# Kernel tuning notes

Hardware: AMD Instinct MI355X
Metric: run time of the kernel (lower is better)

The kernel has to match this reference:

```python
import jax, jax.numpy as jnp
import numpy as np

N = 1_000_000   # total nodes
D = 128         # hidden_dim
B = 1024        # number of graphs (segments)
E = 2_000_000   # edges (unused by forward math, kept for signature fidelity)
EPS = 1e-16     # PyG softmax denominator epsilon


def setup_inputs() -> dict:
    key = jax.random.key(0)
    k1, k2, k3, k4 = jax.random.split(key, 4)
    x = jax.random.normal(k1, (N, D), dtype=jnp.float32)
    edge_index = jax.random.randint(k2, (2, E), 0, N, dtype=jnp.int32)
    batch = jnp.sort(jax.random.randint(k3, (N,), 0, B, dtype=jnp.int32))
    # Linear(hidden_dim, 1) parameters
    W = jax.random.normal(k4, (1, D), dtype=jnp.float32) * (1.0 / np.sqrt(D))
    b = jnp.zeros((1,), dtype=jnp.float32)
    return {"x": x, "edge_index": edge_index, "batch": batch, "W": W, "b": b}


def reference(x, edge_index, batch, W, b):
    # scores = Linear(x).squeeze(-1)  -> [N]
    scores = (x @ W.T + b)[:, 0]
    # pyg_softmax: segment-wise numerically-stable softmax over `batch`
    seg_max = jax.ops.segment_max(scores, batch, num_segments=B)          # [B]
    ex = jnp.exp(scores - seg_max[batch])                                  # [N]
    seg_sum = jax.ops.segment_sum(ex, batch, num_segments=B)              # [B]
    attn = ex / (seg_sum[batch] + EPS)                                     # [N]
    # global_add_pool of attention-weighted features -> [B, D]
    gx = jax.ops.segment_sum(x * attn[:, None], batch, num_segments=B)
    return gx
```

## Files before the change

### kernel.cpp

```cpp
#include <hip/hip_runtime.h>
#include <math.h>


#define DIM 128

__device__ __forceinline__ int lower_bound_i32(const int* __restrict__ a, int n, int key) {
    int lo = 0, hi = n;
    while (lo < hi) {
        int mid = (lo + hi) >> 1;
        if (a[mid] < key) lo = mid + 1; else hi = mid;
    }
    return lo;
}

__global__ __launch_bounds__(256) void gap_online_kernel(
    const float* __restrict__ x,
    const int*   __restrict__ batch,
    const float* __restrict__ W,
    const float* __restrict__ bias,
    float*       __restrict__ out,
    int N)
{
    const int seg  = blockIdx.x;
    const int tid  = threadIdx.x;
    const int wave = tid >> 6;
    const int lane = tid & 63;

    const int start = lower_bound_i32(batch, N, seg);
    const int end   = lower_bound_i32(batch, N, seg + 1);

    const float2 wv = ((const float2*)W)[lane];
    const float  b0 = bias[0];

    float  m   = -INFINITY;
    float  l   = 0.0f;
    float2 acc = make_float2(0.0f, 0.0f);

    for (int r = start + wave; r < end; r += 4) {
        const float2 xv = ((const float2*)(x + (size_t)r * DIM))[lane];

        float s = xv.x * wv.x + xv.y * wv.y;
        #pragma unroll
        for (int off = 32; off > 0; off >>= 1)
            s += __shfl_xor(s, off, 64);
        s += b0;

        const float m_new = fmaxf(m, s);
        const float alpha = __expf(m - m_new);
        const float w     = __expf(s - m_new);
        l     = l * alpha + w;
        acc.x = acc.x * alpha + w * xv.x;
        acc.y = acc.y * alpha + w * xv.y;
        m     = m_new;
    }

    __shared__ float sm[4];
    __shared__ float sl[4];
    __shared__ float sacc[4][DIM];

    sacc[wave][2 * lane]     = acc.x;
    sacc[wave][2 * lane + 1] = acc.y;
    if (lane == 0) { sm[wave] = m; sl[wave] = l; }
    __syncthreads();

    if (tid < DIM) {
        float m_tot = fmaxf(fmaxf(sm[0], sm[1]), fmaxf(sm[2], sm[3]));
        float num = 0.0f, den = 0.0f;
        #pragma unroll
        for (int w = 0; w < 4; ++w) {
            const float a = (sl[w] > 0.0f) ? __expf(sm[w] - m_tot) : 0.0f;
            num += sacc[w][tid] * a;
            den += sl[w] * a;
        }
        out[(size_t)seg * DIM + tid] = (den > 0.0f) ? (num / (den + 1e-16f)) : 0.0f;
    }
}

extern "C" void kernel_launch(void* const* d_in, const int* in_sizes, int n_in,
                              void* d_out, int out_size, void* d_ws, size_t ws_size,
                              hipStream_t stream) {
    const float* x     = (const float*)d_in[0];
    const int*   batch = (const int*)d_in[2];
    const float* W     = (const float*)d_in[3];
    const float* bias  = (const float*)d_in[4];
    float*       out   = (float*)d_out;

    const int N = in_sizes[2];
    const int B = out_size / DIM;

    gap_online_kernel<<<B, 256, 0, stream>>>(x, batch, W, bias, out, N);
}
```

Measured before the change: 749.8 us.

## Precompute segment offsets and use float4 half-wave rows with prefetch

Replaces the per-block binary searches over batch with a separate kernel that writes segment offsets into workspace. The main kernel now has each half-wave handle one row using float4 loads, so a wave covers two rows per step. Each wave processes 8 rows per iteration and register-prefetches the next group to raise memory-level parallelism. The cost is an extra launch plus a pass over batch. The empty-segment guards are removed, with a large negative sentinel used in place of -inf.

```diff
diff --git a/kernel.cpp b/kernel.cpp
--- a/kernel.cpp
+++ b/kernel.cpp
@@ -3,76 +3,117 @@
 
 
 #define DIM 128
+#define NEG_HUGE (-3.0e38f)
 
-__device__ __forceinline__ int lower_bound_i32(const int* __restrict__ a, int n, int key) {
-    int lo = 0, hi = n;
-    while (lo < hi) {
-        int mid = (lo + hi) >> 1;
-        if (a[mid] < key) lo = mid + 1; else hi = mid;
+__global__ void seg_offsets_kernel(const int* __restrict__ batch,
+                                   int* __restrict__ off, int N, int B) {
+    int i = blockIdx.x * blockDim.x + threadIdx.x;
+    if (i >= N) return;
+    int bi = batch[i];
+    int bp = (i == 0) ? -1 : batch[i - 1];
+    for (int s = bp + 1; s <= bi; ++s) off[s] = i;
+    if (i == N - 1) {
+        for (int s = bi + 1; s <= B; ++s) off[s] = N;
     }
-    return lo;
 }
 
 __global__ __launch_bounds__(256) void gap_online_kernel(
     const float* __restrict__ x,
-    const int*   __restrict__ batch,
+    const int*   __restrict__ off,
     const float* __restrict__ W,
     const float* __restrict__ bias,
-    float*       __restrict__ out,
-    int N)
+    float*       __restrict__ out)
 {
     const int seg  = blockIdx.x;
     const int tid  = threadIdx.x;
     const int wave = tid >> 6;
     const int lane = tid & 63;
+    const int half = lane >> 5;
+    const int hl   = lane & 31;
 
-    const int start = lower_bound_i32(batch, N, seg);
-    const int end   = lower_bound_i32(batch, N, seg + 1);
+    const int start = off[seg];
+    const int end   = off[seg + 1];
 
-    const float2 wv = ((const float2*)W)[lane];
+    const float4 wv = ((const float4*)W)[hl];
     const float  b0 = bias[0];
 
-    float  m   = -INFINITY;
-    float  l   = 0.0f;
-    float2 acc = make_float2(0.0f, 0.0f);
+    float  m = NEG_HUGE;
+    float  l = 0.0f;
+    float4 acc = make_float4(0.f, 0.f, 0.f, 0.f);
 
-    for (int r = start + wave; r < end; r += 4) {
-        const float2 xv = ((const float2*)(x + (size_t)r * DIM))[lane];
+    int p = start + wave * 8;
 
-        float s = xv.x * wv.x + xv.y * wv.y;
-        #pragma unroll
-        for (int off = 32; off > 0; off >>= 1)
-            s += __shfl_xor(s, off, 64);
-        s += b0;
-
-        const float m_new = fmaxf(m, s);
-        const float alpha = __expf(m - m_new);
-        const float w     = __expf(s - m_new);
-        l     = l * alpha + w;
-        acc.x = acc.x * alpha + w * xv.x;
-        acc.y = acc.y * alpha + w * xv.y;
-        m     = m_new;
+    float4 xv[4];
+    #pragma unroll
+    for (int k = 0; k < 4; ++k) {
+        int row = p + 2 * k + half;
+        xv[k] = (row < end) ? ((const float4*)(x + (size_t)row * DIM))[hl]
+                            : make_float4(0.f, 0.f, 0.f, 0.f);
     }
 
-    __shared__ float sm[4];
-    __shared__ float sl[4];
-    __shared__ float sacc[4][DIM];
+    for (; p < end; p += 32) {
+        float4 xn[4];
+        #pragma unroll
+        for (int k = 0; k < 4; ++k) {
+            int row = p + 32 + 2 * k + half;
+            xn[k] = (row < end) ? ((const float4*)(x + (size_t)row * DIM))[hl]
+                                : make_float4(0.f, 0.f, 0.f, 0.f);
+        }
 
-    sacc[wave][2 * lane]     = acc.x;
-    sacc[wave][2 * lane + 1] = acc.y;
-    if (lane == 0) { sm[wave] = m; sl[wave] = l; }
+        float s[4];
+        #pragma unroll
+        for (int k = 0; k < 4; ++k)
+            s[k] = xv[k].x * wv.x + xv[k].y * wv.y + xv[k].z * wv.z + xv[k].w * wv.w;
+
+        #pragma unroll
+        for (int offd = 16; offd > 0; offd >>= 1) {
+            #pragma unroll
+            for (int k = 0; k < 4; ++k)
+                s[k] += __shfl_xor(s[k], offd, 64);
+        }
+
+        #pragma unroll
+        for (int k = 0; k < 4; ++k) {
+            int  row   = p + 2 * k + half;
+            bool valid = row < end;
+            float sk    = valid ? (s[k] + b0) : NEG_HUGE;
+            float m_new = fmaxf(m, sk);
+            float alpha = __expf(m - m_new);
+            float w     = valid ? __expf(sk - m_new) : 0.0f;
+            l     = l * alpha + w;
+            acc.x = acc.x * alpha + w * xv[k].x;
+            acc.y = acc.y * alpha + w * xv[k].y;
+            acc.z = acc.z * alpha + w * xv[k].z;
+            acc.w = acc.w * alpha + w * xv[k].w;
+            m     = m_new;
+            xv[k] = xn[k];
+        }
+    }
+
+    __shared__ float sm[8];
+    __shared__ float sl[8];
+    __shared__ float sacc[8][DIM];
+
+    const int sid = wave * 2 + half;
+    sacc[sid][4 * hl + 0] = acc.x;
+    sacc[sid][4 * hl + 1] = acc.y;
+    sacc[sid][4 * hl + 2] = acc.z;
+    sacc[sid][4 * hl + 3] = acc.w;
+    if (hl == 0) { sm[sid] = m; sl[sid] = l; }
     __syncthreads();
 
     if (tid < DIM) {
-        float m_tot = fmaxf(fmaxf(sm[0], sm[1]), fmaxf(sm[2], sm[3]));
+        float m_tot = NEG_HUGE;
+        #pragma unroll
+        for (int h = 0; h < 8; ++h) m_tot = fmaxf(m_tot, sm[h]);
         float num = 0.0f, den = 0.0f;
         #pragma unroll
-        for (int w = 0; w < 4; ++w) {
-            const float a = (sl[w] > 0.0f) ? __expf(sm[w] - m_tot) : 0.0f;
-            num += sacc[w][tid] * a;
-            den += sl[w] * a;
+        for (int h = 0; h < 8; ++h) {
+            float a = __expf(sm[h] - m_tot);
+            num += sacc[h][tid] * a;
+            den += sl[h] * a;
         }
-        out[(size_t)seg * DIM + tid] = (den > 0.0f) ? (num / (den + 1e-16f)) : 0.0f;
+        out[(size_t)seg * DIM + tid] = num / (den + 1e-16f);
     }
 }
 
@@ -88,5 +129,8 @@
     const int N = in_sizes[2];
     const int B = out_size / DIM;
 
-    gap_online_kernel<<<B, 256, 0, stream>>>(x, batch, W, bias, out, N);
+    int* off = (int*)d_ws;
+
+    seg_offsets_kernel<<<(N + 255) / 256, 256, 0, stream>>>(batch, off, N, B);
+    gap_online_kernel<<<B, 256, 0, stream>>>(x, off, W, bias, out);
 }
```

After: 667.1 us. 11.0% less time.
